# Performance work log

Hardware: AMD Instinct MI355X
Metric: run time of the kernel (lower is better)

Reference implementation:

```python
import jax, jax.numpy as jnp
import numpy as np

B, S, D = 4, 2048, 1024  # batch, seq_len, d_model == d_internal


def setup_inputs() -> dict:
    key = jax.random.key(0)
    ks = jax.random.split(key, 7)
    s = 1.0 / np.sqrt(D)  # scale weights so softmax / relu stay in a sane range
    return {
        "input_vecs": jax.random.normal(ks[0], (B, S, D), jnp.float32),
        "Wq": jax.random.normal(ks[1], (D, D), jnp.float32) * s,
        "Wk": jax.random.normal(ks[2], (D, D), jnp.float32) * s,
        "Wv": jax.random.normal(ks[3], (D, D), jnp.float32) * s,
        "W1": jax.random.normal(ks[4], (D, D), jnp.float32) * s,  # linear1: d_internal -> d_model
        "b1": jnp.zeros((D,), jnp.float32),
        "W2": jax.random.normal(ks[5], (D, D), jnp.float32) * s,  # linear2: d_model -> d_internal
        "b2": jnp.zeros((D,), jnp.float32),
    }


def reference(input_vecs, Wq, Wk, Wv, W1, b1, W2, b2):
    d_internal = Wq.shape[1]
    # single-head self-attention: Q,K,V = X @ Wq/Wk/Wv
    q = jnp.einsum("bsd,de->bse", input_vecs, Wq)
    k = jnp.einsum("bsd,de->bse", input_vecs, Wk)
    v = jnp.einsum("bsd,de->bse", input_vecs, Wv)
    scores = jnp.einsum("bqe,bke->bqk", q, k) / jnp.sqrt(jnp.asarray(d_internal, q.dtype))
    attn = jax.nn.softmax(scores, axis=-1)               # [B, S, S]
    attn_out = jnp.einsum("bqk,bke->bqe", attn, v)       # [B, S, D]
    h = attn_out + input_vecs                            # residual 1
    h = jax.nn.relu(h @ W1 + b1)                         # linear1 + relu
    out = h @ W2 + b2 + input_vecs                       # linear2 + residual 2
    return out, attn
```

## Files before the change

### kernel.cpp

```cpp
#include <hip/hip_runtime.h>
#include <hip/hip_bf16.h>

typedef unsigned short u16;
typedef unsigned int   u32;
typedef u16   u16x8 __attribute__((ext_vector_type(8)));
typedef u16   u16x4 __attribute__((ext_vector_type(4)));
typedef __bf16 bf16x8 __attribute__((ext_vector_type(8)));
typedef float f32x4 __attribute__((ext_vector_type(4)));

__device__ __forceinline__ u16 f2bf(float f) {
    u32 u = __float_as_uint(f);
    u = u + 0x7FFFu + ((u >> 16) & 1u);
    return (u16)(u >> 16);
}

__device__ __forceinline__ void gload16(const u16* g, u16* l) {
    __builtin_amdgcn_global_load_lds(
        (const __attribute__((address_space(1))) void*)g,
        (__attribute__((address_space(3))) void*)l,
        16, 0, 0);
}

__global__ __launch_bounds__(256) void cvt_x(const float* __restrict__ X,
                                             u16* __restrict__ Xb) {
    const long i = (long)(blockIdx.x * 256 + threadIdx.x) * 8;
    float4 a = *(const float4*)(X + i);
    float4 b = *(const float4*)(X + i + 4);
    u16x8 r;
    r[0] = f2bf(a.x); r[1] = f2bf(a.y); r[2] = f2bf(a.z); r[3] = f2bf(a.w);
    r[4] = f2bf(b.x); r[5] = f2bf(b.y); r[6] = f2bf(b.z); r[7] = f2bf(b.w);
    *(u16x8*)(Xb + i) = r;
}

__global__ __launch_bounds__(256) void cvt_wT(const float* __restrict__ w0,
                                              const float* __restrict__ w1,
                                              const float* __restrict__ w2,
                                              const float* __restrict__ w3,
                                              const float* __restrict__ w4,
                                              u16* __restrict__ wt) {
    const float* srcs[5] = {w0, w1, w2, w3, w4};
    const float* W = srcs[blockIdx.z];
    u16* WT = wt + (long)blockIdx.z * 1048576;
    __shared__ float t[32][33];
    const int tx = threadIdx.x, ty = threadIdx.y;
    const int n0 = blockIdx.x * 32, k0 = blockIdx.y * 32;
    #pragma unroll
    for (int r = 0; r < 4; ++r)
        t[ty + 8 * r][tx] = W[(long)(k0 + ty + 8 * r) * 1024 + n0 + tx];
    __syncthreads();
    #pragma unroll
    for (int r = 0; r < 4; ++r)
        WT[(long)(n0 + ty + 8 * r) * 1024 + k0 + tx] = f2bf(t[tx][ty + 8 * r]);
}

#define BM 128
#define BN 128
#define BK 32

enum { EPI_BF16 = 0, EPI_VT = 1, EPI_SCALE_F32 = 2, EPI_ADDX_BF16 = 3,
       EPI_BIAS_RELU_BF16 = 4, EPI_BIAS_ADDX_F32 = 5 };

template <int EPI>
__global__ __launch_bounds__(256, 2)
void gemm_bt(const u16* __restrict__ A, const u16* __restrict__ Bt,
             void* __restrict__ Cout, const float* __restrict__ bias,
             const float* __restrict__ Xres,
             const int M, const int N, const int K,
             const long sA, const long sB, const long sC, const long sX,
             const float scale) {
    const int bz = blockIdx.z;
    const u16* Ab = A + (long)bz * sA;
    const u16* Bb = Bt + (long)bz * sB;
    const float* Xr = Xres ? Xres + (long)bz * sX : nullptr;

    const int tid  = threadIdx.x;
    const int lane = tid & 63;
    const int w    = tid >> 6;
    const int wr   = (w >> 1) * 64;
    const int wc   = (w & 1) * 64;
    const int m0   = blockIdx.x * BM;
    const int n0   = blockIdx.y * BN;

    __shared__ __align__(16) u16 As[BM * BK];
    __shared__ __align__(16) u16 Bs[BN * BK];

    f32x4 acc[4][4] = {};

    const u16* Ag = Ab + (long)(m0 + w * 32 + (lane >> 2)) * K + (lane & 3) * 8;
    const u16* Bg = Bb + (long)(n0 + w * 32 + (lane >> 2)) * K + (lane & 3) * 8;
    const long r16A = 16L * K;
    u16* As0 = &As[(w * 32) * BK];
    u16* As1 = &As[(w * 32 + 16) * BK];
    u16* Bs0 = &Bs[(w * 32) * BK];
    u16* Bs1 = &Bs[(w * 32 + 16) * BK];

    const int rbase = lane & 15;
    const int koff  = (lane >> 4) * 8;

    for (int kt = 0; kt < K; kt += BK) {
        gload16(Ag + kt, As0);
        gload16(Ag + kt + r16A, As1);
        gload16(Bg + kt, Bs0);
        gload16(Bg + kt + r16A, Bs1);
        __syncthreads();

        bf16x8 af[4], bfr[4];
        #pragma unroll
        for (int mi = 0; mi < 4; ++mi)
            af[mi] = *(const bf16x8*)(&As[(wr + mi * 16 + rbase) * BK + koff]);
        #pragma unroll
        for (int ni = 0; ni < 4; ++ni)
            bfr[ni] = *(const bf16x8*)(&Bs[(wc + ni * 16 + rbase) * BK + koff]);
        #pragma unroll
        for (int mi = 0; mi < 4; ++mi)
            #pragma unroll
            for (int ni = 0; ni < 4; ++ni)
                acc[mi][ni] = __builtin_amdgcn_mfma_f32_16x16x32_bf16(
                    af[mi], bfr[ni], acc[mi][ni], 0, 0, 0);
        __syncthreads();
    }

    const int colb = wc + (lane & 15);
    const int rq   = (lane >> 4) * 4;
    #pragma unroll
    for (int mi = 0; mi < 4; ++mi) {
        #pragma unroll
        for (int ni = 0; ni < 4; ++ni) {
            f32x4 v = acc[mi][ni];
            const int gr0 = m0 + wr + mi * 16 + rq;
            const int gc  = n0 + colb + ni * 16;
            if constexpr (EPI == EPI_VT) {
                u16x4 p;
                p[0] = f2bf(v[0]); p[1] = f2bf(v[1]);
                p[2] = f2bf(v[2]); p[3] = f2bf(v[3]);
                u16* C = (u16*)Cout;
                const long off = ((long)(gr0 >> 11)) * 2097152 +
                                 (long)gc * 2048 + (gr0 & 2047);
                *(u16x4*)(C + off) = p;
            } else {
                #pragma unroll
                for (int j = 0; j < 4; ++j) {
                    const long idx = (long)(gr0 + j) * N + gc;
                    float val = v[j];
                    if constexpr (EPI == EPI_BF16) {
                        ((u16*)Cout + (long)bz * sC)[idx] = f2bf(val);
                    } else if constexpr (EPI == EPI_SCALE_F32) {
                        ((float*)Cout + (long)bz * sC)[idx] = val * scale;
                    } else if constexpr (EPI == EPI_ADDX_BF16) {
                        val += Xr[idx];
                        ((u16*)Cout + (long)bz * sC)[idx] = f2bf(val);
                    } else if constexpr (EPI == EPI_BIAS_RELU_BF16) {
                        val = fmaxf(val + bias[gc], 0.0f);
                        ((u16*)Cout + (long)bz * sC)[idx] = f2bf(val);
                    } else if constexpr (EPI == EPI_BIAS_ADDX_F32) {
                        ((float*)Cout + (long)bz * sC)[idx] =
                            val + bias[gc] + Xr[idx];
                    }
                }
            }
        }
    }
}

__global__ __launch_bounds__(256)
void softmax_rows(float* __restrict__ attn, u16* __restrict__ P) {
    const int row  = blockIdx.x;
    float* rp      = attn + (long)row * 2048;
    const int tid  = threadIdx.x;
    const int lane = tid & 63;
    const int w    = tid >> 6;

    float4 v0 = *(const float4*)(rp + tid * 8);
    float4 v1 = *(const float4*)(rp + tid * 8 + 4);

    float m = fmaxf(fmaxf(fmaxf(v0.x, v0.y), fmaxf(v0.z, v0.w)),
                    fmaxf(fmaxf(v1.x, v1.y), fmaxf(v1.z, v1.w)));
    #pragma unroll
    for (int o = 32; o > 0; o >>= 1) m = fmaxf(m, __shfl_xor(m, o));
    __shared__ float redm[4];
    if (lane == 0) redm[w] = m;
    __syncthreads();
    m = fmaxf(fmaxf(redm[0], redm[1]), fmaxf(redm[2], redm[3]));

    float e[8];
    e[0] = __expf(v0.x - m); e[1] = __expf(v0.y - m);
    e[2] = __expf(v0.z - m); e[3] = __expf(v0.w - m);
    e[4] = __expf(v1.x - m); e[5] = __expf(v1.y - m);
    e[6] = __expf(v1.z - m); e[7] = __expf(v1.w - m);
    float s = ((e[0] + e[1]) + (e[2] + e[3])) + ((e[4] + e[5]) + (e[6] + e[7]));
    #pragma unroll
    for (int o = 32; o > 0; o >>= 1) s += __shfl_xor(s, o);
    __shared__ float reds[4];
    if (lane == 0) reds[w] = s;
    __syncthreads();
    s = (reds[0] + reds[1]) + (reds[2] + reds[3]);
    const float inv = 1.0f / s;

    float4 o0, o1;
    o0.x = e[0] * inv; o0.y = e[1] * inv; o0.z = e[2] * inv; o0.w = e[3] * inv;
    o1.x = e[4] * inv; o1.y = e[5] * inv; o1.z = e[6] * inv; o1.w = e[7] * inv;
    *(float4*)(rp + tid * 8)     = o0;
    *(float4*)(rp + tid * 8 + 4) = o1;

    u16x8 pb;
    pb[0] = f2bf(o0.x); pb[1] = f2bf(o0.y); pb[2] = f2bf(o0.z); pb[3] = f2bf(o0.w);
    pb[4] = f2bf(o1.x); pb[5] = f2bf(o1.y); pb[6] = f2bf(o1.z); pb[7] = f2bf(o1.w);
    *(u16x8*)(P + (long)row * 2048 + tid * 8) = pb;
}

extern "C" void kernel_launch(void* const* d_in, const int* in_sizes, int n_in,
                              void* d_out, int out_size, void* d_ws, size_t ws_size,
                              hipStream_t stream) {
    const float* X  = (const float*)d_in[0];
    const float* Wq = (const float*)d_in[1];
    const float* Wk = (const float*)d_in[2];
    const float* Wv = (const float*)d_in[3];
    const float* W1 = (const float*)d_in[4];
    const float* b1 = (const float*)d_in[5];
    const float* W2 = (const float*)d_in[6];
    const float* b2 = (const float*)d_in[7];

    float* out  = (float*)d_out;
    float* attn = out + (size_t)8388608;

    char* ws = (char*)d_ws;
    u16* Xb  = (u16*)(ws);
    u16* Qb  = (u16*)(ws + (size_t)16 * 1024 * 1024);
    u16* Kb  = (u16*)(ws + (size_t)32 * 1024 * 1024);
    u16* VT  = (u16*)(ws + (size_t)48 * 1024 * 1024);
    u16* H1b = (u16*)(ws + (size_t)64 * 1024 * 1024);
    u16* WTs = (u16*)(ws + (size_t)80 * 1024 * 1024);
    u16* WqT = WTs + (size_t)0 * 1048576;
    u16* WkT = WTs + (size_t)1 * 1048576;
    u16* WvT = WTs + (size_t)2 * 1048576;
    u16* W1T = WTs + (size_t)3 * 1048576;
    u16* W2T = WTs + (size_t)4 * 1048576;
    u16* Pb  = Xb;
    u16* Hb  = Kb;

    cvt_x<<<4096, 256, 0, stream>>>(X, Xb);
    cvt_wT<<<dim3(32, 32, 5), dim3(32, 8), 0, stream>>>(Wq, Wk, Wv, W1, W2, WTs);

    gemm_bt<EPI_BF16><<<dim3(64, 8, 1), 256, 0, stream>>>(
        Xb, WqT, Qb, nullptr, nullptr, 8192, 1024, 1024, 0, 0, 0, 0, 1.0f);
    gemm_bt<EPI_BF16><<<dim3(64, 8, 1), 256, 0, stream>>>(
        Xb, WkT, Kb, nullptr, nullptr, 8192, 1024, 1024, 0, 0, 0, 0, 1.0f);
    gemm_bt<EPI_VT><<<dim3(64, 8, 1), 256, 0, stream>>>(
        Xb, WvT, VT, nullptr, nullptr, 8192, 1024, 1024, 0, 0, 0, 0, 1.0f);

    gemm_bt<EPI_SCALE_F32><<<dim3(16, 16, 4), 256, 0, stream>>>(
        Qb, Kb, attn, nullptr, nullptr, 2048, 2048, 1024,
        2048L * 1024, 2048L * 1024, 2048L * 2048, 0, 0.03125f);

    softmax_rows<<<8192, 256, 0, stream>>>(attn, Pb);

    gemm_bt<EPI_ADDX_BF16><<<dim3(16, 8, 4), 256, 0, stream>>>(
        Pb, VT, Hb, nullptr, X, 2048, 1024, 2048,
        2048L * 2048, 1024L * 2048, 2048L * 1024, 2048L * 1024, 1.0f);

    gemm_bt<EPI_BIAS_RELU_BF16><<<dim3(64, 8, 1), 256, 0, stream>>>(
        Hb, W1T, H1b, b1, nullptr, 8192, 1024, 1024, 0, 0, 0, 0, 1.0f);

    gemm_bt<EPI_BIAS_ADDX_F32><<<dim3(64, 8, 1), 256, 0, stream>>>(
        H1b, W2T, out, b2, X, 8192, 1024, 1024, 0, 0, 0, 0, 1.0f);
}
```

Measured before the change: 283.1 us.

## Swizzle LDS tile layout and fuse Q/K/V projections into one launch

XORs the 16-byte chunk index with row bits on both the global-to-LDS load and the fragment read, so the MFMA operand reads from shared memory avoid bank conflicts. It also merges the three Q/K/V projection GEMMs into one batched launch over blockIdx.z, picking the output buffer and the V-transpose epilogue by batch index. The merge removes two launches and gives a larger grid per wave, at the cost of a branch in the epilogue.

```diff
diff --git a/kernel.cpp b/kernel.cpp
--- a/kernel.cpp
+++ b/kernel.cpp
@@ -57,14 +57,15 @@
 #define BN 128
 #define BK 32
 
-enum { EPI_BF16 = 0, EPI_VT = 1, EPI_SCALE_F32 = 2, EPI_ADDX_BF16 = 3,
+enum { EPI_QKV = 0, EPI_SCALE_F32 = 2, EPI_ADDX_BF16 = 3,
        EPI_BIAS_RELU_BF16 = 4, EPI_BIAS_ADDX_F32 = 5 };
 
 template <int EPI>
 __global__ __launch_bounds__(256, 2)
 void gemm_bt(const u16* __restrict__ A, const u16* __restrict__ Bt,
-             void* __restrict__ Cout, const float* __restrict__ bias,
-             const float* __restrict__ Xres,
+             void* __restrict__ Cout, void* __restrict__ CoutK,
+             void* __restrict__ CoutV,
+             const float* __restrict__ bias, const float* __restrict__ Xres,
              const int M, const int N, const int K,
              const long sA, const long sB, const long sC, const long sX,
              const float scale) {
@@ -86,8 +87,9 @@
 
     f32x4 acc[4][4] = {};
 
-    const u16* Ag = Ab + (long)(m0 + w * 32 + (lane >> 2)) * K + (lane & 3) * 8;
-    const u16* Bg = Bb + (long)(n0 + w * 32 + (lane >> 2)) * K + (lane & 3) * 8;
+    const int schunk = ((lane & 3) ^ ((lane >> 3) & 3)) * 8;
+    const u16* Ag = Ab + (long)(m0 + w * 32 + (lane >> 2)) * K + schunk;
+    const u16* Bg = Bb + (long)(n0 + w * 32 + (lane >> 2)) * K + schunk;
     const long r16A = 16L * K;
     u16* As0 = &As[(w * 32) * BK];
     u16* As1 = &As[(w * 32 + 16) * BK];
@@ -95,7 +97,7 @@
     u16* Bs1 = &Bs[(w * 32 + 16) * BK];
 
     const int rbase = lane & 15;
-    const int koff  = (lane >> 4) * 8;
+    const int koff  = (((lane >> 4) ^ ((rbase >> 1) & 3))) * 8;
 
     for (int kt = 0; kt < K; kt += BK) {
         gload16(Ag + kt, As0);
@@ -129,22 +131,27 @@
             f32x4 v = acc[mi][ni];
             const int gr0 = m0 + wr + mi * 16 + rq;
             const int gc  = n0 + colb + ni * 16;
-            if constexpr (EPI == EPI_VT) {
-                u16x4 p;
-                p[0] = f2bf(v[0]); p[1] = f2bf(v[1]);
-                p[2] = f2bf(v[2]); p[3] = f2bf(v[3]);
-                u16* C = (u16*)Cout;
-                const long off = ((long)(gr0 >> 11)) * 2097152 +
-                                 (long)gc * 2048 + (gr0 & 2047);
-                *(u16x4*)(C + off) = p;
+            if constexpr (EPI == EPI_QKV) {
+                if (bz == 2) {
+                    u16x4 p;
+                    p[0] = f2bf(v[0]); p[1] = f2bf(v[1]);
+                    p[2] = f2bf(v[2]); p[3] = f2bf(v[3]);
+                    u16* C = (u16*)CoutV;
+                    const long off = ((long)(gr0 >> 11)) * 2097152 +
+                                     (long)gc * 2048 + (gr0 & 2047);
+                    *(u16x4*)(C + off) = p;
+                } else {
+                    u16* C = (u16*)(bz == 0 ? Cout : CoutK);
+                    #pragma unroll
+                    for (int j = 0; j < 4; ++j)
+                        C[(long)(gr0 + j) * N + gc] = f2bf(v[j]);
+                }
             } else {
                 #pragma unroll
                 for (int j = 0; j < 4; ++j) {
                     const long idx = (long)(gr0 + j) * N + gc;
                     float val = v[j];
-                    if constexpr (EPI == EPI_BF16) {
-                        ((u16*)Cout + (long)bz * sC)[idx] = f2bf(val);
-                    } else if constexpr (EPI == EPI_SCALE_F32) {
+                    if constexpr (EPI == EPI_SCALE_F32) {
                         ((float*)Cout + (long)bz * sC)[idx] = val * scale;
                     } else if constexpr (EPI == EPI_ADDX_BF16) {
                         val += Xr[idx];
@@ -230,9 +237,6 @@
     u16* VT  = (u16*)(ws + (size_t)48 * 1024 * 1024);
     u16* H1b = (u16*)(ws + (size_t)64 * 1024 * 1024);
     u16* WTs = (u16*)(ws + (size_t)80 * 1024 * 1024);
-    u16* WqT = WTs + (size_t)0 * 1048576;
-    u16* WkT = WTs + (size_t)1 * 1048576;
-    u16* WvT = WTs + (size_t)2 * 1048576;
     u16* W1T = WTs + (size_t)3 * 1048576;
     u16* W2T = WTs + (size_t)4 * 1048576;
     u16* Pb  = Xb;
@@ -241,26 +245,25 @@
     cvt_x<<<4096, 256, 0, stream>>>(X, Xb);
     cvt_wT<<<dim3(32, 32, 5), dim3(32, 8), 0, stream>>>(Wq, Wk, Wv, W1, W2, WTs);
 
-    gemm_bt<EPI_BF16><<<dim3(64, 8, 1), 256, 0, stream>>>(
-        Xb, WqT, Qb, nullptr, nullptr, 8192, 1024, 1024, 0, 0, 0, 0, 1.0f);
-    gemm_bt<EPI_BF16><<<dim3(64, 8, 1), 256, 0, stream>>>(
-        Xb, WkT, Kb, nullptr, nullptr, 8192, 1024, 1024, 0, 0, 0, 0, 1.0f);
-    gemm_bt<EPI_VT><<<dim3(64, 8, 1), 256, 0, stream>>>(
-        Xb, WvT, VT, nullptr, nullptr, 8192, 1024, 1024, 0, 0, 0, 0, 1.0f);
+    gemm_bt<EPI_QKV><<<dim3(64, 8, 3), 256, 0, stream>>>(
+        Xb, WTs, Qb, Kb, VT, nullptr, nullptr, 8192, 1024, 1024,
+        0, 1048576, 0, 0, 1.0f);
 
     gemm_bt<EPI_SCALE_F32><<<dim3(16, 16, 4), 256, 0, stream>>>(
-        Qb, Kb, attn, nullptr, nullptr, 2048, 2048, 1024,
+        Qb, Kb, attn, nullptr, nullptr, nullptr, nullptr, 2048, 2048, 1024,
         2048L * 1024, 2048L * 1024, 2048L * 2048, 0, 0.03125f);
 
     softmax_rows<<<8192, 256, 0, stream>>>(attn, Pb);
 
     gemm_bt<EPI_ADDX_BF16><<<dim3(16, 8, 4), 256, 0, stream>>>(
-        Pb, VT, Hb, nullptr, X, 2048, 1024, 2048,
+        Pb, VT, Hb, nullptr, nullptr, nullptr, X, 2048, 1024, 2048,
         2048L * 2048, 1024L * 2048, 2048L * 1024, 2048L * 1024, 1.0f);
 
     gemm_bt<EPI_BIAS_RELU_BF16><<<dim3(64, 8, 1), 256, 0, stream>>>(
-        Hb, W1T, H1b, b1, nullptr, 8192, 1024, 1024, 0, 0, 0, 0, 1.0f);
+        Hb, W1T, H1b, nullptr, nullptr, b1, nullptr, 8192, 1024, 1024,
+        0, 0, 0, 0, 1.0f);
 
     gemm_bt<EPI_BIAS_ADDX_F32><<<dim3(64, 8, 1), 256, 0, stream>>>(
-        H1b, W2T, out, b2, X, 8192, 1024, 1024, 0, 0, 0, 0, 1.0f);
-}
+        H1b, W2T, out, nullptr, nullptr, b2, X, 8192, 1024, 1024,
+        0, 0, 0, 0, 1.0f);
+}
```

Measured after the change: 266.5 us. 5.9% less time.
